# Performance work log

Hardware: AMD Instinct MI355X
Metric: run time of the kernel (lower is better)

The kernel has to match this reference:

```python
import jax, jax.numpy as jnp
import numpy as np

N_GRAPHS = 128  # number of graphs in the batch (max value of `batch`)
NEG_SLOPE = 0.2  # PyG GATConv default LeakyReLU slope


def gat_conv(x, src, dst, W, att_src, att_dst, bias, concat):
    """PyG-style GATConv (eval mode). x: [N, F_in]; src/dst: [E] (self-loops included)."""
    N = x.shape[0]
    H, C = att_src.shape
    xh = (x @ W).reshape(N, H, C)                      # [N, H, C]
    a_src = jnp.sum(xh * att_src, axis=-1)             # [N, H]
    a_dst = jnp.sum(xh * att_dst, axis=-1)             # [N, H]
    alpha = a_src[src] + a_dst[dst]                    # [E, H] edge scores
    alpha = jax.nn.leaky_relu(alpha, NEG_SLOPE)
    # segment softmax over incoming edges of each dst node
    amax = jax.ops.segment_max(alpha, dst, num_segments=N)   # [N, H]
    e = jnp.exp(alpha - amax[dst])                            # [E, H]
    denom = jax.ops.segment_sum(e, dst, num_segments=N)      # [N, H]
    attn = e / denom[dst]                                     # [E, H]
    msg = xh[src] * attn[:, :, None]                          # [E, H, C]
    out = jax.ops.segment_sum(msg, dst, num_segments=N)      # [N, H, C]
    out = out.reshape(N, H * C) if concat else out.mean(axis=1)
    return out + bias


def setup_inputs():
    key = jax.random.key(0)
    ks = jax.random.split(key, 12)
    N, E, F_in, H, C_hid, C_out = 50000, 800000, 128, 8, 32, 10
    x = jax.random.normal(ks[0], (N, F_in), dtype=jnp.float32)
    edge_index = jax.random.randint(ks[1], (2, E), 0, N, dtype=jnp.int32)
    batch = jnp.sort(jax.random.randint(ks[2], (N,), 0, N_GRAPHS, dtype=jnp.int32))
    s_in = 1.0 / np.sqrt(F_in)
    s_h = 1.0 / np.sqrt(H * C_hid)
    W1 = jax.random.normal(ks[3], (F_in, H * C_hid), dtype=jnp.float32) * s_in
    att_src1 = jax.random.normal(ks[4], (H, C_hid), dtype=jnp.float32) * 0.1
    att_dst1 = jax.random.normal(ks[5], (H, C_hid), dtype=jnp.float32) * 0.1
    b1 = jnp.zeros((H * C_hid,), dtype=jnp.float32)
    W2 = jax.random.normal(ks[6], (H * C_hid, C_out), dtype=jnp.float32) * s_h
    att_src2 = jax.random.normal(ks[7], (1, C_out), dtype=jnp.float32) * 0.1
    att_dst2 = jax.random.normal(ks[8], (1, C_out), dtype=jnp.float32) * 0.1
    b2 = jnp.zeros((C_out,), dtype=jnp.float32)
    return {"x": x, "edge_index": edge_index, "batch": batch,
            "W1": W1, "att_src1": att_src1, "att_dst1": att_dst1, "b1": b1,
            "W2": W2, "att_src2": att_src2, "att_dst2": att_dst2, "b2": b2}


def reference(x, edge_index, batch, W1, att_src1, att_dst1, b1, W2, att_src2, att_dst2, b2):
    N = x.shape[0]
    # PyG GATConv default: add self-loops
    loops = jnp.arange(N, dtype=edge_index.dtype)
    src = jnp.concatenate([edge_index[0], loops])
    dst = jnp.concatenate([edge_index[1], loops])
    # eval mode: dropout(p=0.6) is identity
    h = gat_conv(x, src, dst, W1, att_src1, att_dst1, b1, concat=True)   # [N, H*C_hid]
    h = jax.nn.elu(h)
    h = gat_conv(h, src, dst, W2, att_src2, att_dst2, b2, concat=False)  # [N, C_out]
    h = jax.nn.elu(h)
    # global mean pool over graphs
    sums = jax.ops.segment_sum(h, batch, num_segments=N_GRAPHS)          # [G, C_out]
    counts = jax.ops.segment_sum(jnp.ones((N,), h.dtype), batch, num_segments=N_GRAPHS)
    pooled = sums / jnp.maximum(counts, 1.0)[:, None]
    return jax.nn.log_softmax(pooled, axis=1)
```

## Files before the change

### kernel.cpp

```cpp
#include <hip/hip_runtime.h>

#define N_NODES 50000
#define N_EDGES 800000
#define E_TOT   850000
#define F_IN    128
#define HC      256
#define NH      8
#define C_OUT   10
#define N_GRAPH 128
#define NBLK    49
#define XSTRIDE 16
#define NB_DEG  3322

typedef __attribute__((ext_vector_type(8))) short bf16x8;
typedef __attribute__((ext_vector_type(4))) float f32x4;

__device__ __forceinline__ float lrelu(float x){ return x > 0.f ? x : 0.2f * x; }
__device__ __forceinline__ float elu1(float x){ return x > 0.f ? x : (__expf(x) - 1.f); }

__device__ __forceinline__ unsigned short f2bf(float f){
    unsigned int u = __float_as_uint(f);
    return (unsigned short)((u + 0x7fffu + ((u >> 16) & 1u)) >> 16);
}
__device__ __forceinline__ float bf2f(unsigned short h){
    return __uint_as_float((unsigned int)h << 16);
}
__device__ __forceinline__ void unp2(unsigned int p, float& a, float& b){
    a = __uint_as_float(p << 16);
    b = __uint_as_float(p & 0xffff0000u);
}

__global__ void k_setup(const int* __restrict__ ei, int* __restrict__ deg,
                        const float* __restrict__ W1, unsigned short* __restrict__ bt,
                        const float* __restrict__ W2, float* __restrict__ W2t){
    int b = blockIdx.x;
    if (b < NB_DEG){
        int e = b * 256 + threadIdx.x;
        if (e < E_TOT){
            int dst = (e < N_EDGES) ? ei[N_EDGES + e] : (e - N_EDGES);
            atomicAdd(deg + dst, 1);
        }
    } else if (b < NB_DEG + 128){
        int k = b - NB_DEG;
        int c = threadIdx.x;
        float v = W1[k * HC + c];
        unsigned short hi = f2bf(v);
        unsigned short lo = f2bf(v - bf2f(hi));
        bt[(size_t)c * 256 + k]       = hi;
        bt[(size_t)c * 256 + 128 + k] = lo;
    } else {
        for (int j = threadIdx.x; j < HC * C_OUT; j += 256){
            int k = j / C_OUT, c = j % C_OUT;
            W2t[c * HC + k] = W2[j];
        }
    }
}

__global__ __launch_bounds__(256) void k_gemm1m(const float* __restrict__ x,
                                                const unsigned short* __restrict__ bt,
                                                const float* __restrict__ atts,
                                                const float* __restrict__ attd,
                                                unsigned short* __restrict__ xhb,
                                                float* __restrict__ a_s,
                                                float* __restrict__ a_d){
    __shared__ unsigned short tile[4][32][264];
    __shared__ float sc[4][32][8], dc[4][32][8];
    const int wave = threadIdx.x >> 6, lane = threadIdx.x & 63;
    const int quad = lane >> 4, lidx = lane & 15;
    const int m0 = blockIdx.x * 128 + wave * 32;
    int ar0 = m0 + lidx;      if (ar0 >= N_NODES) ar0 = N_NODES - 1;
    int ar1 = m0 + 16 + lidx; if (ar1 >= N_NODES) ar1 = N_NODES - 1;

    bf16x8 ah0[4], al0[4], ah1[4], al1[4];
    #pragma unroll
    for (int ks = 0; ks < 4; ks++){
        const float* p0 = x + (size_t)ar0 * F_IN + ks * 32 + quad * 8;
        const float* p1 = x + (size_t)ar1 * F_IN + ks * 32 + quad * 8;
        float4 u0 = *(const float4*)p0, u1 = *(const float4*)(p0 + 4);
        float4 w0 = *(const float4*)p1, w1 = *(const float4*)(p1 + 4);
        float v0[8] = {u0.x,u0.y,u0.z,u0.w,u1.x,u1.y,u1.z,u1.w};
        float v1[8] = {w0.x,w0.y,w0.z,w0.w,w1.x,w1.y,w1.z,w1.w};
        bf16x8 h0v, l0v, h1v, l1v;
        #pragma unroll
        for (int j = 0; j < 8; j++){
            unsigned short hh = f2bf(v0[j]);
            h0v[j] = (short)hh;
            l0v[j] = (short)f2bf(v0[j] - bf2f(hh));
            unsigned short hg = f2bf(v1[j]);
            h1v[j] = (short)hg;
            l1v[j] = (short)f2bf(v1[j] - bf2f(hg));
        }
        ah0[ks] = h0v; al0[ks] = l0v; ah1[ks] = h1v; al1[ks] = l1v;
    }

    const uint4* bbase = (const uint4*)bt;
    for (int h = 0; h < NH; h++){
        float ss0[4] = {0,0,0,0}, ss1[4] = {0,0,0,0};
        float dd0[4] = {0,0,0,0}, dd1[4] = {0,0,0,0};
        #pragma unroll
        for (int sub = 0; sub < 2; sub++){
            int col = h * 32 + sub * 16 + lidx;
            const uint4* bcol = bbase + (size_t)col * 32 + quad;
            bf16x8 bh[4], bl[4];
            #pragma unroll
            for (int ks = 0; ks < 4; ks++){
                bh[ks] = __builtin_bit_cast(bf16x8, bcol[ks * 4]);
                bl[ks] = __builtin_bit_cast(bf16x8, bcol[16 + ks * 4]);
            }
            f32x4 acc0 = {0.f,0.f,0.f,0.f}, acc1 = {0.f,0.f,0.f,0.f};
            #pragma unroll
            for (int ks = 0; ks < 4; ks++){
                acc0 = __builtin_amdgcn_mfma_f32_16x16x32_bf16(ah0[ks], bh[ks], acc0, 0, 0, 0);
                acc1 = __builtin_amdgcn_mfma_f32_16x16x32_bf16(ah1[ks], bh[ks], acc1, 0, 0, 0);
            }
            #pragma unroll
            for (int ks = 0; ks < 4; ks++){
                acc0 = __builtin_amdgcn_mfma_f32_16x16x32_bf16(ah0[ks], bl[ks], acc0, 0, 0, 0);
                acc1 = __builtin_amdgcn_mfma_f32_16x16x32_bf16(ah1[ks], bl[ks], acc1, 0, 0, 0);
            }
            #pragma unroll
            for (int ks = 0; ks < 4; ks++){
                acc0 = __builtin_amdgcn_mfma_f32_16x16x32_bf16(al0[ks], bh[ks], acc0, 0, 0, 0);
                acc1 = __builtin_amdgcn_mfma_f32_16x16x32_bf16(al1[ks], bh[ks], acc1, 0, 0, 0);
            }
            float sv = atts[col], dv = attd[col];
            #pragma unroll
            for (int reg = 0; reg < 4; reg++){
                tile[wave][quad*4+reg][col]    = f2bf(acc0[reg]);
                tile[wave][16+quad*4+reg][col] = f2bf(acc1[reg]);
                ss0[reg] += acc0[reg] * sv;  dd0[reg] += acc0[reg] * dv;
                ss1[reg] += acc1[reg] * sv;  dd1[reg] += acc1[reg] * dv;
            }
        }
        #pragma unroll
        for (int reg = 0; reg < 4; reg++){
            float a = ss0[reg], b = dd0[reg], c = ss1[reg], d = dd1[reg];
            a += __shfl_xor(a,1,64); a += __shfl_xor(a,2,64); a += __shfl_xor(a,4,64); a += __shfl_xor(a,8,64);
            b += __shfl_xor(b,1,64); b += __shfl_xor(b,2,64); b += __shfl_xor(b,4,64); b += __shfl_xor(b,8,64);
            c += __shfl_xor(c,1,64); c += __shfl_xor(c,2,64); c += __shfl_xor(c,4,64); c += __shfl_xor(c,8,64);
            d += __shfl_xor(d,1,64); d += __shfl_xor(d,2,64); d += __shfl_xor(d,4,64); d += __shfl_xor(d,8,64);
            if (lidx == 0){
                sc[wave][quad*4+reg][h]    = a;  dc[wave][quad*4+reg][h]    = b;
                sc[wave][16+quad*4+reg][h] = c;  dc[wave][16+quad*4+reg][h] = d;
            }
        }
    }
    __syncthreads();
    for (int r = 0; r < 32; r++){
        int row = m0 + r;
        if (row < N_NODES){
            uint2 p = *(const uint2*)&tile[wave][r][lane * 4];
            ((uint2*)xhb)[(size_t)row * 64 + lane] = p;
        }
    }
    {
        int linear = lane * 4;
        int row = m0 + (linear >> 3);
        if (row < N_NODES){
            const float* sb = &sc[wave][0][0];
            const float* db = &dc[wave][0][0];
            float4 s4 = *(const float4*)(sb + linear);
            float4 d4 = *(const float4*)(db + linear);
            *(float4*)(a_s + (size_t)m0 * NH + linear) = s4;
            *(float4*)(a_d + (size_t)m0 * NH + linear) = d4;
        }
    }
}

__global__ void k_bsum(const int* __restrict__ deg, int* __restrict__ bsum){
    int b = blockIdx.x;
    int v = 0;
    for (int i = threadIdx.x; i < 1024; i += 256){
        int idx = b * 1024 + i;
        if (idx < N_NODES) v += deg[idx];
    }
    #pragma unroll
    for (int off = 1; off < 64; off <<= 1) v += __shfl_xor(v, off, 64);
    __shared__ int sd[4];
    if ((threadIdx.x & 63) == 0) sd[threadIdx.x >> 6] = v;
    __syncthreads();
    if (threadIdx.x == 0) bsum[b] = sd[0] + sd[1] + sd[2] + sd[3];
}

__global__ void k_scanb(const int* __restrict__ bsum, int* __restrict__ bexcl, int* __restrict__ rowp){
    int l = threadIdx.x;
    int v = (l < NBLK) ? bsum[l] : 0;
    int incl = v;
    #pragma unroll
    for (int off = 1; off < 64; off <<= 1){
        int t = __shfl_up(incl, off, 64);
        if (l >= off) incl += t;
    }
    if (l < NBLK) bexcl[l] = incl - v;
    if (l == 0) rowp[N_NODES] = E_TOT;
}

__global__ __launch_bounds__(1024) void k_scan(const int* __restrict__ deg, const int* __restrict__ bexcl,
                                               int* __restrict__ rowp, int* __restrict__ cur){
    __shared__ int sd[1024];
    int b = blockIdx.x;
    int i = b * 1024 + threadIdx.x;
    int v = (i < N_NODES) ? deg[i] : 0;
    sd[threadIdx.x] = v;
    __syncthreads();
    for (int off = 1; off < 1024; off <<= 1){
        int t = (threadIdx.x >= off) ? sd[threadIdx.x - off] : 0;
        __syncthreads();
        sd[threadIdx.x] += t;
        __syncthreads();
    }
    if (i < N_NODES){
        int excl = sd[threadIdx.x] - v + bexcl[b];
        rowp[i] = excl;
        cur[i]  = excl;
    }
}

__global__ void k_scatter(const int* __restrict__ ei, int* __restrict__ cur, int* __restrict__ col){
    int e = blockIdx.x * 256 + threadIdx.x;
    if (e >= E_TOT) return;
    int s, d;
    if (e < N_EDGES){ s = ei[e]; d = ei[N_EDGES + e]; }
    else { s = e - N_EDGES; d = s; }
    int slot = atomicAdd(cur + d, 1);
    col[slot] = s;
}

__global__ __launch_bounds__(256) void k_agg1f(const unsigned short* __restrict__ xhb,
                                               const float* __restrict__ a_s, const float* __restrict__ a_d,
                                               const int* __restrict__ rowp, const int* __restrict__ colb,
                                               const float* __restrict__ b1, const float* __restrict__ W2t,
                                               const float* __restrict__ as2, const float* __restrict__ ad2,
                                               float* __restrict__ xh2){
    int wave = threadIdx.x >> 6, lane = threadIdx.x & 63;
    int n = blockIdx.x * 4 + wave;
    if (n >= N_NODES) return;
    int h = lane >> 3;
    float adh = a_d[(unsigned)(n * NH + h)];
    int s0 = rowp[n], s1 = rowp[n + 1];
    const uint2* xv = (const uint2*)xhb;
    float ax0=0.f, ay0=0.f, az0=0.f, aw0=0.f, den0=0.f;
    float ax1=0.f, ay1=0.f, az1=0.f, aw1=0.f, den1=0.f;
    int idx = s0;
    for (; idx + 1 < s1; idx += 2){
        int sA = colb[idx], sB = colb[idx + 1];
        float aA = a_s[(unsigned)(sA * NH + h)];
        float aB = a_s[(unsigned)(sB * NH + h)];
        uint2 pA = xv[(unsigned)(sA * 64 + lane)];
        uint2 pB = xv[(unsigned)(sB * 64 + lane)];
        float wA = __expf(lrelu(aA + adh));
        float wB = __expf(lrelu(aB + adh));
        den0 += wA; den1 += wB;
        float v0, v1, v2, v3;
        unp2(pA.x, v0, v1); unp2(pA.y, v2, v3);
        ax0 += wA*v0; ay0 += wA*v1; az0 += wA*v2; aw0 += wA*v3;
        unp2(pB.x, v0, v1); unp2(pB.y, v2, v3);
        ax1 += wB*v0; ay1 += wB*v1; az1 += wB*v2; aw1 += wB*v3;
    }
    if (idx < s1){
        int sA = colb[idx];
        float wA = __expf(lrelu(a_s[(unsigned)(sA * NH + h)] + adh));
        den0 += wA;
        uint2 pA = xv[(unsigned)(sA * 64 + lane)];
        float v0, v1, v2, v3;
        unp2(pA.x, v0, v1); unp2(pA.y, v2, v3);
        ax0 += wA*v0; ay0 += wA*v1; az0 += wA*v2; aw0 += wA*v3;
    }
    float rden = 1.f / (den0 + den1);
    float4 bb = ((const float4*)b1)[lane];
    float4 r;
    r.x = elu1((ax0 + ax1) * rden + bb.x);
    r.y = elu1((ay0 + ay1) * rden + bb.y);
    r.z = elu1((az0 + az1) * rden + bb.z);
    r.w = elu1((aw0 + aw1) * rden + bb.w);
    float o[C_OUT];
    #pragma unroll
    for (int c = 0; c < C_OUT; c++){
        float4 w = ((const float4*)(W2t + c * HC))[lane];
        float v = r.x*w.x + r.y*w.y + r.z*w.z + r.w*w.w;
        v += __shfl_xor(v, 1, 64); v += __shfl_xor(v, 2, 64); v += __shfl_xor(v, 4, 64);
        v += __shfl_xor(v, 8, 64); v += __shfl_xor(v, 16, 64); v += __shfl_xor(v, 32, 64);
        o[c] = v;
    }
    if (lane == 0){
        float s2 = 0.f, d2 = 0.f;
        #pragma unroll
        for (int c = 0; c < C_OUT; c++){ s2 += o[c] * as2[c]; d2 += o[c] * ad2[c]; }
        float* xr = xh2 + (unsigned)(n * XSTRIDE);
        *(float4*)(xr)     = make_float4(o[0], o[1], o[2], o[3]);
        *(float4*)(xr + 4) = make_float4(o[4], o[5], o[6], o[7]);
        *(float4*)(xr + 8) = make_float4(o[8], o[9], s2, d2);
    }
}

__global__ __launch_bounds__(256) void k_agg2(const float* __restrict__ xh2,
                                              const int* __restrict__ rowp, const int* __restrict__ colb,
                                              const float* __restrict__ b2,
                                              float* __restrict__ h2){
    int grp = threadIdx.x >> 4, l16 = threadIdx.x & 15;
    int n = blockIdx.x * 16 + grp;
    if (n >= N_NODES) return;
    float adn = xh2[(unsigned)(n * XSTRIDE + 11)];
    int s0 = rowp[n], s1 = rowp[n + 1];
    float acc[C_OUT] = {};
    float den = 0.f;
    for (int idx = s0 + l16; idx < s1; idx += 16){
        int s = colb[idx];
        const float* xr = xh2 + (unsigned)(s * XSTRIDE);
        float4 q0 = *(const float4*)(xr);
        float4 q1 = *(const float4*)(xr + 4);
        float4 q2 = *(const float4*)(xr + 8);
        float w = __expf(lrelu(q2.z + adn));
        den += w;
        acc[0] += w*q0.x; acc[1] += w*q0.y; acc[2] += w*q0.z; acc[3] += w*q0.w;
        acc[4] += w*q1.x; acc[5] += w*q1.y; acc[6] += w*q1.z; acc[7] += w*q1.w;
        acc[8] += w*q2.x; acc[9] += w*q2.y;
    }
    #pragma unroll
    for (int off = 1; off < 16; off <<= 1){
        den += __shfl_xor(den, off, 64);
        #pragma unroll
        for (int c = 0; c < C_OUT; c++) acc[c] += __shfl_xor(acc[c], off, 64);
    }
    if (l16 == 0){
        float rden = 1.f / den;
        #pragma unroll
        for (int c = 0; c < C_OUT; c++)
            h2[(unsigned)(n * C_OUT + c)] = elu1(acc[c] * rden + b2[c]);
    }
}

__global__ __launch_bounds__(256) void k_pool(const float* __restrict__ h2, const int* __restrict__ batch,
                                              float* __restrict__ out){
    int g = blockIdx.x;
    int l = 0, r = N_NODES;
    while (l < r){ int m = (l + r) >> 1; if (batch[m] < g) l = m + 1; else r = m; }
    int lo = l;
    l = 0; r = N_NODES;
    while (l < r){ int m = (l + r) >> 1; if (batch[m] < g + 1) l = m + 1; else r = m; }
    int hi = l;
    float acc[C_OUT] = {};
    for (int i = lo + (int)threadIdx.x; i < hi; i += 256){
        const float* row = h2 + (size_t)i * C_OUT;
        #pragma unroll
        for (int c = 0; c < C_OUT; c++) acc[c] += row[c];
    }
    #pragma unroll
    for (int c = 0; c < C_OUT; c++){
        #pragma unroll
        for (int off = 32; off > 0; off >>= 1) acc[c] += __shfl_xor(acc[c], off, 64);
    }
    __shared__ float sd[4][C_OUT];
    int wave = threadIdx.x >> 6, lane = threadIdx.x & 63;
    if (lane == 0){
        #pragma unroll
        for (int c = 0; c < C_OUT; c++) sd[wave][c] = acc[c];
    }
    __syncthreads();
    if (threadIdx.x == 0){
        float cnt = (float)(hi - lo);
        if (cnt < 1.f) cnt = 1.f;
        float v[C_OUT];
        float m = -1e30f;
        #pragma unroll
        for (int c = 0; c < C_OUT; c++){
            v[c] = (sd[0][c] + sd[1][c] + sd[2][c] + sd[3][c]) / cnt;
            m = fmaxf(m, v[c]);
        }
        float sum = 0.f;
        #pragma unroll
        for (int c = 0; c < C_OUT; c++) sum += __expf(v[c] - m);
        float lse = m + __logf(sum);
        #pragma unroll
        for (int c = 0; c < C_OUT; c++) out[g * C_OUT + c] = v[c] - lse;
    }
}

extern "C" void kernel_launch(void* const* d_in, const int* in_sizes, int n_in,
                              void* d_out, int out_size, void* d_ws, size_t ws_size,
                              hipStream_t stream){
    const float* x    = (const float*)d_in[0];
    const int*   ei   = (const int*)d_in[1];
    const int*   batch= (const int*)d_in[2];
    const float* W1   = (const float*)d_in[3];
    const float* as1  = (const float*)d_in[4];
    const float* ad1  = (const float*)d_in[5];
    const float* b1   = (const float*)d_in[6];
    const float* W2   = (const float*)d_in[7];
    const float* as2v = (const float*)d_in[8];
    const float* ad2v = (const float*)d_in[9];
    const float* b2   = (const float*)d_in[10];
    float* out = (float*)d_out;

    char* ws = (char*)d_ws;
    size_t off = 0;
    auto alloc = [&](size_t bytes)->char*{
        char* p = ws + off;
        off = (off + bytes + 255) & ~(size_t)255;
        return p;
    };
    unsigned short* xhb  = (unsigned short*)alloc((size_t)N_NODES * HC * 2);
    unsigned short* bt   = (unsigned short*)alloc((size_t)HC * 256 * 2);
    float* asc1 = (float*)alloc((size_t)N_NODES * NH * 4);
    float* adc1 = (float*)alloc((size_t)N_NODES * NH * 4);
    int*   deg  = (int*)alloc((size_t)N_NODES * 4);
    int*   rowp = (int*)alloc((size_t)(N_NODES + 1) * 4);
    int*   cur  = (int*)alloc((size_t)N_NODES * 4);
    int*   colb = (int*)alloc((size_t)E_TOT * 4);
    int*   bsum = (int*)alloc(64 * 4);
    int*   bexcl= (int*)alloc(64 * 4);
    float* xh2  = (float*)alloc((size_t)N_NODES * XSTRIDE * 4);
    float* W2t  = (float*)alloc((size_t)HC * C_OUT * 4);
    float* h2   = (float*)alloc((size_t)N_NODES * C_OUT * 4);
    (void)ws_size; (void)in_sizes; (void)n_in; (void)out_size;

    hipMemsetAsync(deg, 0, (size_t)N_NODES * 4, stream);
    hipLaunchKernelGGL(k_setup,   dim3(NB_DEG + 129), dim3(256), 0, stream, ei, deg, W1, bt, W2, W2t);
    hipLaunchKernelGGL(k_gemm1m,  dim3(391),   dim3(256), 0, stream, x, bt, as1, ad1, xhb, asc1, adc1);
    hipLaunchKernelGGL(k_bsum,    dim3(NBLK),  dim3(256), 0, stream, deg, bsum);
    hipLaunchKernelGGL(k_scanb,   dim3(1),     dim3(64),  0, stream, bsum, bexcl, rowp);
    hipLaunchKernelGGL(k_scan,    dim3(NBLK),  dim3(1024),0, stream, deg, bexcl, rowp, cur);
    hipLaunchKernelGGL(k_scatter, dim3((E_TOT + 255)/256), dim3(256), 0, stream, ei, cur, colb);
    hipLaunchKernelGGL(k_agg1f,   dim3((N_NODES + 3)/4), dim3(256), 0, stream, xhb, asc1, adc1, rowp, colb, b1, W2t, as2v, ad2v, xh2);
    hipLaunchKernelGGL(k_agg2,    dim3((N_NODES + 15)/16), dim3(256), 0, stream, xh2, rowp, colb, b2, h2);
    hipLaunchKernelGGL(k_pool,    dim3(N_GRAPH), dim3(256), 0, stream, h2, batch, out);
}
```

Measured before the change: 320.7 us.

## Split GEMM1 heads across two blocks, stream per-head stores, unroll agg1 by four

The first GEMM kernel now launches twice as many blocks, each computing four of the eight heads for a 128-row tile. This raises parallelism on the many-CU device and shrinks the shared-memory tile, so occupancy can go up. Each head's 32 columns are written out right after they are computed instead of through one large staging tile. The cost is that each block now converts the x rows to bf16 twice as often. Separately, the layer-1 aggregation loop is unrolled from two to four edges per iteration to expose more memory-level parallelism on the gathers.

```diff
diff --git a/kernel.cpp b/kernel.cpp
--- a/kernel.cpp
+++ b/kernel.cpp
@@ -63,11 +63,13 @@
                                                 unsigned short* __restrict__ xhb,
                                                 float* __restrict__ a_s,
                                                 float* __restrict__ a_d){
-    __shared__ unsigned short tile[4][32][264];
-    __shared__ float sc[4][32][8], dc[4][32][8];
+    __shared__ unsigned short ht[4][32][40];
+    __shared__ float sc[4][32][4], dc[4][32][4];
     const int wave = threadIdx.x >> 6, lane = threadIdx.x & 63;
     const int quad = lane >> 4, lidx = lane & 15;
-    const int m0 = blockIdx.x * 128 + wave * 32;
+    const int bid = blockIdx.x;
+    const int m0 = (bid >> 1) * 128 + wave * 32;
+    const int hbase = (bid & 1) * 4;
     int ar0 = m0 + lidx;      if (ar0 >= N_NODES) ar0 = N_NODES - 1;
     int ar1 = m0 + 16 + lidx; if (ar1 >= N_NODES) ar1 = N_NODES - 1;
 
@@ -94,7 +96,8 @@
     }
 
     const uint4* bbase = (const uint4*)bt;
-    for (int h = 0; h < NH; h++){
+    for (int hh = 0; hh < 4; hh++){
+        const int h = hbase + hh;
         float ss0[4] = {0,0,0,0}, ss1[4] = {0,0,0,0};
         float dd0[4] = {0,0,0,0}, dd1[4] = {0,0,0,0};
         #pragma unroll
@@ -124,12 +127,23 @@
                 acc1 = __builtin_amdgcn_mfma_f32_16x16x32_bf16(al1[ks], bh[ks], acc1, 0, 0, 0);
             }
             float sv = atts[col], dv = attd[col];
+            int lcol = sub * 16 + lidx;
             #pragma unroll
             for (int reg = 0; reg < 4; reg++){
-                tile[wave][quad*4+reg][col]    = f2bf(acc0[reg]);
-                tile[wave][16+quad*4+reg][col] = f2bf(acc1[reg]);
+                ht[wave][quad*4+reg][lcol]    = f2bf(acc0[reg]);
+                ht[wave][16+quad*4+reg][lcol] = f2bf(acc1[reg]);
                 ss0[reg] += acc0[reg] * sv;  dd0[reg] += acc0[reg] * dv;
                 ss1[reg] += acc1[reg] * sv;  dd1[reg] += acc1[reg] * dv;
+            }
+        }
+        {
+            int row = lane >> 1, half = lane & 1;
+            int globrow = m0 + row;
+            if (globrow < N_NODES){
+                const uint4* src = (const uint4*)&ht[wave][row][half * 16];
+                uint4* dst = (uint4*)(xhb + (size_t)globrow * HC + h * 32 + half * 16);
+                dst[0] = src[0];
+                dst[1] = src[1];
             }
         }
         #pragma unroll
@@ -140,29 +154,19 @@
             c += __shfl_xor(c,1,64); c += __shfl_xor(c,2,64); c += __shfl_xor(c,4,64); c += __shfl_xor(c,8,64);
             d += __shfl_xor(d,1,64); d += __shfl_xor(d,2,64); d += __shfl_xor(d,4,64); d += __shfl_xor(d,8,64);
             if (lidx == 0){
-                sc[wave][quad*4+reg][h]    = a;  dc[wave][quad*4+reg][h]    = b;
-                sc[wave][16+quad*4+reg][h] = c;  dc[wave][16+quad*4+reg][h] = d;
-            }
-        }
-    }
-    __syncthreads();
-    for (int r = 0; r < 32; r++){
-        int row = m0 + r;
-        if (row < N_NODES){
-            uint2 p = *(const uint2*)&tile[wave][r][lane * 4];
-            ((uint2*)xhb)[(size_t)row * 64 + lane] = p;
+                sc[wave][quad*4+reg][hh]    = a;  dc[wave][quad*4+reg][hh]    = b;
+                sc[wave][16+quad*4+reg][hh] = c;  dc[wave][16+quad*4+reg][hh] = d;
+            }
         }
     }
     {
-        int linear = lane * 4;
-        int row = m0 + (linear >> 3);
-        if (row < N_NODES){
-            const float* sb = &sc[wave][0][0];
-            const float* db = &dc[wave][0][0];
-            float4 s4 = *(const float4*)(sb + linear);
-            float4 d4 = *(const float4*)(db + linear);
-            *(float4*)(a_s + (size_t)m0 * NH + linear) = s4;
-            *(float4*)(a_d + (size_t)m0 * NH + linear) = d4;
+        int row = lane >> 1, pair = lane & 1;
+        int globrow = m0 + row;
+        if (globrow < N_NODES){
+            float2 s2 = *(const float2*)&sc[wave][row][pair * 2];
+            float2 d2 = *(const float2*)&dc[wave][row][pair * 2];
+            *(float2*)(a_s + (size_t)globrow * NH + hbase + pair * 2) = s2;
+            *(float2*)(a_d + (size_t)globrow * NH + hbase + pair * 2) = d2;
         }
     }
 }
@@ -242,22 +246,32 @@
     float ax0=0.f, ay0=0.f, az0=0.f, aw0=0.f, den0=0.f;
     float ax1=0.f, ay1=0.f, az1=0.f, aw1=0.f, den1=0.f;
     int idx = s0;
-    for (; idx + 1 < s1; idx += 2){
-        int sA = colb[idx], sB = colb[idx + 1];
+    for (; idx + 3 < s1; idx += 4){
+        int sA = colb[idx], sB = colb[idx+1], sC = colb[idx+2], sD = colb[idx+3];
         float aA = a_s[(unsigned)(sA * NH + h)];
         float aB = a_s[(unsigned)(sB * NH + h)];
+        float aC = a_s[(unsigned)(sC * NH + h)];
+        float aD = a_s[(unsigned)(sD * NH + h)];
         uint2 pA = xv[(unsigned)(sA * 64 + lane)];
         uint2 pB = xv[(unsigned)(sB * 64 + lane)];
+        uint2 pC = xv[(unsigned)(sC * 64 + lane)];
+        uint2 pD = xv[(unsigned)(sD * 64 + lane)];
         float wA = __expf(lrelu(aA + adh));
         float wB = __expf(lrelu(aB + adh));
-        den0 += wA; den1 += wB;
+        float wC = __expf(lrelu(aC + adh));
+        float wD = __expf(lrelu(aD + adh));
+        den0 += wA + wC; den1 += wB + wD;
         float v0, v1, v2, v3;
         unp2(pA.x, v0, v1); unp2(pA.y, v2, v3);
         ax0 += wA*v0; ay0 += wA*v1; az0 += wA*v2; aw0 += wA*v3;
         unp2(pB.x, v0, v1); unp2(pB.y, v2, v3);
         ax1 += wB*v0; ay1 += wB*v1; az1 += wB*v2; aw1 += wB*v3;
-    }
-    if (idx < s1){
+        unp2(pC.x, v0, v1); unp2(pC.y, v2, v3);
+        ax0 += wC*v0; ay0 += wC*v1; az0 += wC*v2; aw0 += wC*v3;
+        unp2(pD.x, v0, v1); unp2(pD.y, v2, v3);
+        ax1 += wD*v0; ay1 += wD*v1; az1 += wD*v2; aw1 += wD*v3;
+    }
+    for (; idx < s1; idx++){
         int sA = colb[idx];
         float wA = __expf(lrelu(a_s[(unsigned)(sA * NH + h)] + adh));
         den0 += wA;
@@ -416,7 +430,7 @@
 
     hipMemsetAsync(deg, 0, (size_t)N_NODES * 4, stream);
     hipLaunchKernelGGL(k_setup,   dim3(NB_DEG + 129), dim3(256), 0, stream, ei, deg, W1, bt, W2, W2t);
-    hipLaunchKernelGGL(k_gemm1m,  dim3(391),   dim3(256), 0, stream, x, bt, as1, ad1, xhb, asc1, adc1);
+    hipLaunchKernelGGL(k_gemm1m,  dim3(782),   dim3(256), 0, stream, x, bt, as1, ad1, xhb, asc1, adc1);
     hipLaunchKernelGGL(k_bsum,    dim3(NBLK),  dim3(256), 0, stream, deg, bsum);
     hipLaunchKernelGGL(k_scanb,   dim3(1),     dim3(64),  0, stream, bsum, bexcl, rowp);
     hipLaunchKernelGGL(k_scan,    dim3(NBLK),  dim3(1024),0, stream, deg, bexcl, rowp, cur);
```

New measurement: 325.6 us. No clear change (+1.5%).

## Cooperatively compute edge weights in layer-1 aggregation and split MFMA accumulator chains

Applied to the files above, without the earlier changes.

In the layer-1 aggregation kernel, each wave now loads 8 neighbor indices and computes all 8x8 head attention weights in parallel, one per lane, then broadcasts them with shuffles. Previously every lane redundantly computed an exp for its own head on each edge, with serially dependent index and score loads. Separately, the bf16 hi/lo split GEMM now accumulates into three independent MFMA chains that are summed at the end, which shortens the dependency chain between MFMAs. The cost is extra shuffles, more accumulator registers and a single accumulator chain in the aggregation loop.

```diff
diff --git a/kernel.cpp b/kernel.cpp
--- a/kernel.cpp
+++ b/kernel.cpp
@@ -107,21 +107,22 @@
                 bh[ks] = __builtin_bit_cast(bf16x8, bcol[ks * 4]);
                 bl[ks] = __builtin_bit_cast(bf16x8, bcol[16 + ks * 4]);
             }
-            f32x4 acc0 = {0.f,0.f,0.f,0.f}, acc1 = {0.f,0.f,0.f,0.f};
+            f32x4 a0A = {0.f,0.f,0.f,0.f}, a0B = {0.f,0.f,0.f,0.f}, a0C = {0.f,0.f,0.f,0.f};
+            f32x4 a1A = {0.f,0.f,0.f,0.f}, a1B = {0.f,0.f,0.f,0.f}, a1C = {0.f,0.f,0.f,0.f};
             #pragma unroll
             for (int ks = 0; ks < 4; ks++){
-                acc0 = __builtin_amdgcn_mfma_f32_16x16x32_bf16(ah0[ks], bh[ks], acc0, 0, 0, 0);
-                acc1 = __builtin_amdgcn_mfma_f32_16x16x32_bf16(ah1[ks], bh[ks], acc1, 0, 0, 0);
+                a0A = __builtin_amdgcn_mfma_f32_16x16x32_bf16(ah0[ks], bh[ks], a0A, 0, 0, 0);
+                a1A = __builtin_amdgcn_mfma_f32_16x16x32_bf16(ah1[ks], bh[ks], a1A, 0, 0, 0);
+                a0B = __builtin_amdgcn_mfma_f32_16x16x32_bf16(ah0[ks], bl[ks], a0B, 0, 0, 0);
+                a1B = __builtin_amdgcn_mfma_f32_16x16x32_bf16(ah1[ks], bl[ks], a1B, 0, 0, 0);
+                a0C = __builtin_amdgcn_mfma_f32_16x16x32_bf16(al0[ks], bh[ks], a0C, 0, 0, 0);
+                a1C = __builtin_amdgcn_mfma_f32_16x16x32_bf16(al1[ks], bh[ks], a1C, 0, 0, 0);
             }
+            f32x4 acc0, acc1;
             #pragma unroll
-            for (int ks = 0; ks < 4; ks++){
-                acc0 = __builtin_amdgcn_mfma_f32_16x16x32_bf16(ah0[ks], bl[ks], acc0, 0, 0, 0);
-                acc1 = __builtin_amdgcn_mfma_f32_16x16x32_bf16(ah1[ks], bl[ks], acc1, 0, 0, 0);
-            }
-            #pragma unroll
-            for (int ks = 0; ks < 4; ks++){
-                acc0 = __builtin_amdgcn_mfma_f32_16x16x32_bf16(al0[ks], bh[ks], acc0, 0, 0, 0);
-                acc1 = __builtin_amdgcn_mfma_f32_16x16x32_bf16(al1[ks], bh[ks], acc1, 0, 0, 0);
+            for (int reg = 0; reg < 4; reg++){
+                acc0[reg] = (a0A[reg] + a0B[reg]) + a0C[reg];
+                acc1[reg] = (a1A[reg] + a1B[reg]) + a1C[reg];
             }
             float sv = atts[col], dv = attd[col];
             #pragma unroll
@@ -236,43 +237,44 @@
     int n = blockIdx.x * 4 + wave;
     if (n >= N_NODES) return;
     int h = lane >> 3;
+    int hw = lane & 7;
     float adh = a_d[(unsigned)(n * NH + h)];
+    float adw = a_d[(unsigned)(n * NH + hw)];
     int s0 = rowp[n], s1 = rowp[n + 1];
     const uint2* xv = (const uint2*)xhb;
-    float ax0=0.f, ay0=0.f, az0=0.f, aw0=0.f, den0=0.f;
-    float ax1=0.f, ay1=0.f, az1=0.f, aw1=0.f, den1=0.f;
+    float ax = 0.f, ay = 0.f, az = 0.f, aw = 0.f, den = 0.f;
     int idx = s0;
-    for (; idx + 1 < s1; idx += 2){
-        int sA = colb[idx], sB = colb[idx + 1];
-        float aA = a_s[(unsigned)(sA * NH + h)];
-        float aB = a_s[(unsigned)(sB * NH + h)];
-        uint2 pA = xv[(unsigned)(sA * 64 + lane)];
-        uint2 pB = xv[(unsigned)(sB * 64 + lane)];
-        float wA = __expf(lrelu(aA + adh));
-        float wB = __expf(lrelu(aB + adh));
-        den0 += wA; den1 += wB;
-        float v0, v1, v2, v3;
-        unp2(pA.x, v0, v1); unp2(pA.y, v2, v3);
-        ax0 += wA*v0; ay0 += wA*v1; az0 += wA*v2; aw0 += wA*v3;
-        unp2(pB.x, v0, v1); unp2(pB.y, v2, v3);
-        ax1 += wB*v0; ay1 += wB*v1; az1 += wB*v2; aw1 += wB*v3;
-    }
-    if (idx < s1){
+    for (; idx + 7 < s1; idx += 8){
+        int sj = colb[idx + (lane >> 3)];
+        float wj = __expf(lrelu(a_s[(unsigned)(sj * NH + hw)] + adw));
+        #pragma unroll
+        for (int j = 0; j < 8; j++){
+            int srcl = j * 8 + h;
+            float w = __shfl(wj, srcl, 64);
+            int s   = __shfl(sj, srcl, 64);
+            den += w;
+            uint2 p = xv[(unsigned)(s * 64 + lane)];
+            float v0, v1, v2, v3;
+            unp2(p.x, v0, v1); unp2(p.y, v2, v3);
+            ax += w*v0; ay += w*v1; az += w*v2; aw += w*v3;
+        }
+    }
+    for (; idx < s1; idx++){
         int sA = colb[idx];
         float wA = __expf(lrelu(a_s[(unsigned)(sA * NH + h)] + adh));
-        den0 += wA;
+        den += wA;
         uint2 pA = xv[(unsigned)(sA * 64 + lane)];
         float v0, v1, v2, v3;
         unp2(pA.x, v0, v1); unp2(pA.y, v2, v3);
-        ax0 += wA*v0; ay0 += wA*v1; az0 += wA*v2; aw0 += wA*v3;
-    }
-    float rden = 1.f / (den0 + den1);
+        ax += wA*v0; ay += wA*v1; az += wA*v2; aw += wA*v3;
+    }
+    float rden = 1.f / den;
     float4 bb = ((const float4*)b1)[lane];
     float4 r;
-    r.x = elu1((ax0 + ax1) * rden + bb.x);
-    r.y = elu1((ay0 + ay1) * rden + bb.y);
-    r.z = elu1((az0 + az1) * rden + bb.z);
-    r.w = elu1((aw0 + aw1) * rden + bb.w);
+    r.x = elu1(ax * rden + bb.x);
+    r.y = elu1(ay * rden + bb.y);
+    r.z = elu1(az * rden + bb.z);
+    r.w = elu1(aw * rden + bb.w);
     float o[C_OUT];
     #pragma unroll
     for (int c = 0; c < C_OUT; c++){
```

Result: no change. 318.1 us (-0.8%).
